# Optimization experiments

Measured on AMD Instinct MI355X. Metric: run time of the kernel, lower is better.

Reference implementation:

```python
import jax, jax.numpy as jnp
import numpy as np

B, N = 256, 256


def greedy_hard_perm(soft_perm):
    # soft_perm: (B, N, N). Sequential greedy masked-argmax assignment, vectorized over batch.
    Bn, Nn, _ = soft_perm.shape
    NEG = jnp.finfo(soft_perm.dtype).min
    b_idx = jnp.arange(Bn)

    def step(carry, _):
        scores, hard, row_mask, col_mask = carry
        # mask out already-assigned rows/cols (in-place masked_fill_ in torch -> carried scores)
        scores = jnp.where(row_mask[:, :, None], NEG, scores)
        scores = jnp.where(col_mask[:, None, :], NEG, scores)
        flat_idx = jnp.argmax(scores.reshape(Bn, -1), axis=1)  # (B,)
        r = flat_idx // Nn
        c = flat_idx % Nn
        hard = hard.at[b_idx, r, c].set(1.0)
        row_mask = row_mask.at[b_idx, r].set(True)
        col_mask = col_mask.at[b_idx, c].set(True)
        return (scores, hard, row_mask, col_mask), None

    init = (
        soft_perm,
        jnp.zeros_like(soft_perm),
        jnp.zeros((Bn, Nn), dtype=bool),
        jnp.zeros((Bn, Nn), dtype=bool),
    )
    (_, hard, _, _), _ = jax.lax.scan(step, init, None, length=Nn)
    return hard


def setup_inputs() -> dict:
    key = jax.random.key(0)
    logits = jax.random.normal(key, (B, N, N), dtype=jnp.float32)
    # realistic soft permutation: row-stochastic scores
    soft_perm = jax.nn.softmax(logits, axis=-1)
    return {"soft_perm": soft_perm}


def reference(soft_perm):
    # hard perm carries no gradient (built from constant 1.0 writes in torch)
    hard = greedy_hard_perm(jax.lax.stop_gradient(soft_perm))
    # straight-through estimator: forward = hard, backward = identity through soft
    return hard + soft_perm - jax.lax.stop_gradient(soft_perm)
```

## Files before the change

### kernel.cpp

```cpp
#include <hip/hip_runtime.h>
#include <math.h>

#define NEGINF (-INFINITY)

template <int CTRL>
__device__ __forceinline__ float dppmax(float x) {
    int xi = __float_as_int(x);
    int yi = __builtin_amdgcn_update_dpp(xi, xi, CTRL, 0xf, 0xf, false);
    return fmaxf(x, __int_as_float(yi));
}

__device__ __forceinline__ float wave_max64(float x) {
    x = dppmax<0x111>(x);
    x = dppmax<0x112>(x);
    x = dppmax<0x114>(x);
    x = dppmax<0x118>(x);
    x = dppmax<0x142>(x);
    x = dppmax<0x143>(x);
    return __int_as_float(__builtin_amdgcn_readlane(__float_as_int(x), 63));
}

__device__ __forceinline__ void wave_argmax(float v, int idx, float& out_v, int& out_idx) {
    float mv = wave_max64(v);
    unsigned long long mask = __ballot(v == mv);
    int ln = (int)__builtin_ctzll(mask);
    int bi = __builtin_amdgcn_readlane(idx, ln);
    unsigned long long rest = mask & (mask - 1);
    if (rest) {
        while (rest) {
            int l2 = (int)__builtin_ctzll(rest); rest &= rest - 1;
            int b2 = __builtin_amdgcn_readlane(idx, l2);
            if (b2 < bi) bi = b2;
        }
    }
    out_v = mv; out_idx = bi;
}

__global__ __launch_bounds__(64, 1) void greedy_perm_kernel(
        const float* __restrict__ soft, float* __restrict__ out) {
    const int b = blockIdx.x;
    const int lane = threadIdx.x;
    const size_t base = (size_t)b << 16;
    const float* sc = soft + base;
    float* ob = out + base;

    float v[4];
    int   c[4];

#pragma unroll
    for (int j = 0; j < 4; ++j) { v[j] = NEGINF; c[j] = 0; }

    const float4 zero4 = make_float4(0.f, 0.f, 0.f, 0.f);

    for (int k = 0; k < 64; k += 4) {
        float4 w[4][4];
#pragma unroll
        for (int j = 0; j < 4; ++j) {
            const float4* rp = (const float4*)(sc + (size_t)(j * 64 + lane) * 256);
#pragma unroll
            for (int kk = 0; kk < 4; ++kk) w[j][kk] = rp[k + kk];
        }
#pragma unroll
        for (int j = 0; j < 4; ++j) {
            float4* op = (float4*)(ob + (size_t)(j * 64 + lane) * 256);
#pragma unroll
            for (int kk = 0; kk < 4; ++kk) op[k + kk] = zero4;
        }
#pragma unroll
        for (int j = 0; j < 4; ++j) {
#pragma unroll
            for (int kk = 0; kk < 4; ++kk) {
                const float4 ww = w[j][kk];
                const int bc = 4 * (k + kk);
                if (ww.x > v[j]) { v[j] = ww.x; c[j] = bc + 0; }
                if (ww.y > v[j]) { v[j] = ww.y; c[j] = bc + 1; }
                if (ww.z > v[j]) { v[j] = ww.z; c[j] = bc + 2; }
                if (ww.w > v[j]) { v[j] = ww.w; c[j] = bc + 3; }
            }
        }
    }

    __threadfence_block();

    unsigned int colmask = 0;

    for (int step = 0; step < 256; ++step) {
        float bv = v[0];
        int   bf = (lane << 8) | (c[0] & 255);
#pragma unroll
        for (int j = 1; j < 4; ++j) {
            int f = ((j * 64 + lane) << 8) | (c[j] & 255);
            if (v[j] > bv || (v[j] == bv && f < bf)) { bv = v[j]; bf = f; }
        }
        float gv; int gf;
        wave_argmax(bv, bf, gv, gf);
        const int r  = gf >> 8;
        const int cc = gf & 255;

        if (lane == 0) ob[gf] = 1.0f;
        if (lane == (r & 63)) { v[r >> 6] = NEGINF; c[r >> 6] = 300; }
        if (lane == (cc >> 2)) colmask |= 1u << (cc & 3);

#pragma unroll
        for (int j = 0; j < 4; ++j) {
            unsigned long long m = __ballot(c[j] == cc);
            while (m) {
                const int ln = (int)__builtin_ctzll(m); m &= m - 1;
                const int row = j * 64 + ln;
                float4 w = *(const float4*)(sc + (size_t)row * 256 + lane * 4);
                float m0 = (colmask & 1u) ? NEGINF : w.x;
                float m1 = (colmask & 2u) ? NEGINF : w.y;
                float m2 = (colmask & 4u) ? NEGINF : w.z;
                float m3 = (colmask & 8u) ? NEGINF : w.w;
                float lv = m0; int lf = 4 * lane + 0;
                if (m1 > lv) { lv = m1; lf = 4 * lane + 1; }
                if (m2 > lv) { lv = m2; lf = 4 * lane + 2; }
                if (m3 > lv) { lv = m3; lf = 4 * lane + 3; }
                float rv; int rf;
                wave_argmax(lv, lf, rv, rf);
                if (lane == ln) { v[j] = rv; c[j] = rf; }
            }
        }
    }
}

extern "C" void kernel_launch(void* const* d_in, const int* in_sizes, int n_in,
                              void* d_out, int out_size, void* d_ws, size_t ws_size,
                              hipStream_t stream) {
    const float* soft = (const float*)d_in[0];
    float* out = (float*)d_out;
    const int n_batches = in_sizes[0] >> 16;

    greedy_perm_kernel<<<n_batches, 64, 0, stream>>>(soft, out);
}
```

Measured before the change: 327.7 us.

## Cache top-2 per row to skip rescans when best column is taken

```diff
diff --git a/kernel.cpp b/kernel.cpp
--- a/kernel.cpp
+++ b/kernel.cpp
@@ -2,6 +2,7 @@
 #include <math.h>
 
 #define NEGINF (-INFINITY)
+#define SENT 300
 
 template <int CTRL>
 __device__ __forceinline__ float dppmax(float x) {
@@ -38,17 +39,15 @@
 
 __global__ __launch_bounds__(64, 1) void greedy_perm_kernel(
         const float* __restrict__ soft, float* __restrict__ out) {
-    const int b = blockIdx.x;
     const int lane = threadIdx.x;
-    const size_t base = (size_t)b << 16;
+    const size_t base = (size_t)blockIdx.x << 16;
     const float* sc = soft + base;
     float* ob = out + base;
 
-    float v[4];
-    int   c[4];
-
+    float v1[4], v2[4];
+    int   c1[4], c2[4];
 #pragma unroll
-    for (int j = 0; j < 4; ++j) { v[j] = NEGINF; c[j] = 0; }
+    for (int j = 0; j < 4; ++j) { v1[j] = NEGINF; c1[j] = 0; v2[j] = NEGINF; c2[j] = 0; }
 
     const float4 zero4 = make_float4(0.f, 0.f, 0.f, 0.f);
 
@@ -71,54 +70,96 @@
 #pragma unroll
             for (int kk = 0; kk < 4; ++kk) {
                 const float4 ww = w[j][kk];
-                const int bc = 4 * (k + kk);
-                if (ww.x > v[j]) { v[j] = ww.x; c[j] = bc + 0; }
-                if (ww.y > v[j]) { v[j] = ww.y; c[j] = bc + 1; }
-                if (ww.z > v[j]) { v[j] = ww.z; c[j] = bc + 2; }
-                if (ww.w > v[j]) { v[j] = ww.w; c[j] = bc + 3; }
+                const float e[4] = {ww.x, ww.y, ww.z, ww.w};
+#pragma unroll
+                for (int q = 0; q < 4; ++q) {
+                    const float wv = e[q];
+                    const int   x  = 4 * (k + kk) + q;
+                    if (wv > v1[j])      { v2[j] = v1[j]; c2[j] = c1[j]; v1[j] = wv; c1[j] = x; }
+                    else if (wv > v2[j]) { v2[j] = wv; c2[j] = x; }
+                }
             }
         }
     }
-
     __threadfence_block();
 
-    unsigned int colmask = 0;
+    unsigned long long cm0 = 0, cm1 = 0, cm2 = 0, cm3 = 0;
 
     for (int step = 0; step < 256; ++step) {
-        float bv = v[0];
-        int   bf = (lane << 8) | (c[0] & 255);
+        float bv = v1[0]; int bf = (lane << 8) | (c1[0] & 255);
 #pragma unroll
         for (int j = 1; j < 4; ++j) {
-            int f = ((j * 64 + lane) << 8) | (c[j] & 255);
-            if (v[j] > bv || (v[j] == bv && f < bf)) { bv = v[j]; bf = f; }
+            int f = ((j * 64 + lane) << 8) | (c1[j] & 255);
+            if (v1[j] > bv || (v1[j] == bv && f < bf)) { bv = v1[j]; bf = f; }
         }
         float gv; int gf;
         wave_argmax(bv, bf, gv, gf);
-        const int r  = gf >> 8;
-        const int cc = gf & 255;
+        const int r = gf >> 8, cc = gf & 255;
 
-        if (lane == 0) ob[gf] = 1.0f;
-        if (lane == (r & 63)) { v[r >> 6] = NEGINF; c[r >> 6] = 300; }
-        if (lane == (cc >> 2)) colmask |= 1u << (cc & 3);
+        if (lane == 0) ob[(size_t)gf] = 1.0f;
+
+        {
+            const unsigned long long bit = 1ull << (cc & 63);
+            const int wsel = cc >> 6;
+            if (wsel == 0) cm0 |= bit; else if (wsel == 1) cm1 |= bit;
+            else if (wsel == 2) cm2 |= bit; else cm3 |= bit;
+        }
+#pragma unroll
+        for (int j = 0; j < 4; ++j)
+            if (r == j * 64 + lane) { v1[j] = NEGINF; c1[j] = SENT; v2[j] = NEGINF; c2[j] = SENT; }
+
+        unsigned need = 0;
+#pragma unroll
+        for (int j = 0; j < 4; ++j) {
+            if (c1[j] == cc) {
+                bool ok = false;
+                const int cx = c2[j];
+                if (cx != SENT) {
+                    const int ws = cx >> 6;
+                    const unsigned long long cw = ws == 0 ? cm0 : ws == 1 ? cm1 : ws == 2 ? cm2 : cm3;
+                    ok = ((cw >> (cx & 63)) & 1ull) == 0;
+                }
+                if (ok) { v1[j] = v2[j]; c1[j] = cx; v2[j] = NEGINF; c2[j] = SENT; }
+                else    need |= 1u << j;
+            }
+        }
 
 #pragma unroll
         for (int j = 0; j < 4; ++j) {
-            unsigned long long m = __ballot(c[j] == cc);
+            unsigned long long m = __ballot((need >> j) & 1u);
             while (m) {
                 const int ln = (int)__builtin_ctzll(m); m &= m - 1;
                 const int row = j * 64 + ln;
                 float4 w = *(const float4*)(sc + (size_t)row * 256 + lane * 4);
-                float m0 = (colmask & 1u) ? NEGINF : w.x;
-                float m1 = (colmask & 2u) ? NEGINF : w.y;
-                float m2 = (colmask & 4u) ? NEGINF : w.z;
-                float m3 = (colmask & 8u) ? NEGINF : w.w;
+                const int wsel = lane >> 4;
+                const unsigned long long cw = wsel == 0 ? cm0 : wsel == 1 ? cm1 : wsel == 2 ? cm2 : cm3;
+                const unsigned nib = (unsigned)(cw >> ((lane & 15) * 4)) & 15u;
+                float m0 = (nib & 1u) ? NEGINF : w.x;
+                float m1 = (nib & 2u) ? NEGINF : w.y;
+                float m2 = (nib & 4u) ? NEGINF : w.z;
+                float m3 = (nib & 8u) ? NEGINF : w.w;
                 float lv = m0; int lf = 4 * lane + 0;
                 if (m1 > lv) { lv = m1; lf = 4 * lane + 1; }
                 if (m2 > lv) { lv = m2; lf = 4 * lane + 2; }
                 if (m3 > lv) { lv = m3; lf = 4 * lane + 3; }
-                float rv; int rf;
-                wave_argmax(lv, lf, rv, rf);
-                if (lane == ln) { v[j] = rv; c[j] = rf; }
+                float rv1; int rf1;
+                wave_argmax(lv, lf, rv1, rf1);
+                if ((rf1 >> 2) == lane) {
+                    const int q = rf1 & 3;
+                    if (q == 0) m0 = NEGINF; else if (q == 1) m1 = NEGINF;
+                    else if (q == 2) m2 = NEGINF; else m3 = NEGINF;
+                }
+                lv = m0; lf = 4 * lane + 0;
+                if (m1 > lv) { lv = m1; lf = 4 * lane + 1; }
+                if (m2 > lv) { lv = m2; lf = 4 * lane + 2; }
+                if (m3 > lv) { lv = m3; lf = 4 * lane + 3; }
+                float rv2; int rf2;
+                wave_argmax(lv, lf, rv2, rf2);
+                if (lane == ln) {
+                    v1[j] = rv1; c1[j] = rf1;
+                    if (rv2 == NEGINF) { v2[j] = NEGINF; c2[j] = SENT; }
+                    else               { v2[j] = rv2;    c2[j] = rf2;  }
+                }
             }
         }
     }
@@ -130,6 +171,5 @@
     const float* soft = (const float*)d_in[0];
     float* out = (float*)d_out;
     const int n_batches = in_sizes[0] >> 16;
-
     greedy_perm_kernel<<<n_batches, 64, 0, stream>>>(soft, out);
 }
```

New measurement: 431.1 us. 31.6% more time.

## Defer stale-row rescans so row reloads overlap the next argmax step

Applied to the files above, without the earlier changes.

```diff
diff --git a/kernel.cpp b/kernel.cpp
--- a/kernel.cpp
+++ b/kernel.cpp
@@ -2,6 +2,8 @@
 #include <math.h>
 
 #define NEGINF (-INFINITY)
+#define C_STALE 256
+#define C_DEAD  511
 
 template <int CTRL>
 __device__ __forceinline__ float dppmax(float x) {
@@ -36,19 +38,34 @@
     out_v = mv; out_idx = bi;
 }
 
+__device__ __forceinline__ void consume_row(int row, float4 b, unsigned colmask,
+                                            int lane, float (&v1)[4], int (&c1)[4]) {
+    float m0 = (colmask & 1u) ? NEGINF : b.x;
+    float m1 = (colmask & 2u) ? NEGINF : b.y;
+    float m2 = (colmask & 4u) ? NEGINF : b.z;
+    float m3 = (colmask & 8u) ? NEGINF : b.w;
+    float lv = m0; int lf = 4 * lane + 0;
+    if (m1 > lv) { lv = m1; lf = 4 * lane + 1; }
+    if (m2 > lv) { lv = m2; lf = 4 * lane + 2; }
+    if (m3 > lv) { lv = m3; lf = 4 * lane + 3; }
+    float rv; int rf;
+    wave_argmax(lv, lf, rv, rf);
+    const int ow = row & 63, jj = row >> 6;
+#pragma unroll
+    for (int j2 = 0; j2 < 4; ++j2)
+        if (j2 == jj && lane == ow) { v1[j2] = rv; c1[j2] = rf; }
+}
+
 __global__ __launch_bounds__(64, 1) void greedy_perm_kernel(
         const float* __restrict__ soft, float* __restrict__ out) {
-    const int b = blockIdx.x;
     const int lane = threadIdx.x;
-    const size_t base = (size_t)b << 16;
+    const size_t base = (size_t)blockIdx.x << 16;
     const float* sc = soft + base;
     float* ob = out + base;
 
-    float v[4];
-    int   c[4];
-
+    float v1[4]; int c1[4];
 #pragma unroll
-    for (int j = 0; j < 4; ++j) { v[j] = NEGINF; c[j] = 0; }
+    for (int j = 0; j < 4; ++j) { v1[j] = NEGINF; c1[j] = 0; }
 
     const float4 zero4 = make_float4(0.f, 0.f, 0.f, 0.f);
 
@@ -72,54 +89,72 @@
             for (int kk = 0; kk < 4; ++kk) {
                 const float4 ww = w[j][kk];
                 const int bc = 4 * (k + kk);
-                if (ww.x > v[j]) { v[j] = ww.x; c[j] = bc + 0; }
-                if (ww.y > v[j]) { v[j] = ww.y; c[j] = bc + 1; }
-                if (ww.z > v[j]) { v[j] = ww.z; c[j] = bc + 2; }
-                if (ww.w > v[j]) { v[j] = ww.w; c[j] = bc + 3; }
+                if (ww.x > v1[j]) { v1[j] = ww.x; c1[j] = bc + 0; }
+                if (ww.y > v1[j]) { v1[j] = ww.y; c1[j] = bc + 1; }
+                if (ww.z > v1[j]) { v1[j] = ww.z; c1[j] = bc + 2; }
+                if (ww.w > v1[j]) { v1[j] = ww.w; c1[j] = bc + 3; }
             }
         }
     }
-
     __threadfence_block();
 
-    unsigned int colmask = 0;
+    unsigned colmask = 0;
+    int nstale = 0, srow0 = 0, srow1 = 0, srow2 = 0;
+    float4 b0 = zero4, b1 = zero4, b2 = zero4;
+    const int lsh = lane << 9;
 
     for (int step = 0; step < 256; ++step) {
-        float bv = v[0];
-        int   bf = (lane << 8) | (c[0] & 255);
+        float gv; int gf;
+        for (;;) {
+            float bv = v1[0]; int bf = lsh | c1[0];
 #pragma unroll
-        for (int j = 1; j < 4; ++j) {
-            int f = ((j * 64 + lane) << 8) | (c[j] & 255);
-            if (v[j] > bv || (v[j] == bv && f < bf)) { bv = v[j]; bf = f; }
+            for (int j = 1; j < 4; ++j) {
+                int f = (j << 15) | lsh | c1[j];
+                if (v1[j] > bv || (v1[j] == bv && f < bf)) { bv = v1[j]; bf = f; }
+            }
+            wave_argmax(bv, bf, gv, gf);
+            if ((gf & 511) != C_STALE) break;
+            if (nstale >= 1) consume_row(srow0, b0, colmask, lane, v1, c1);
+            if (nstale >= 2) consume_row(srow1, b1, colmask, lane, v1, c1);
+            if (nstale >= 3) consume_row(srow2, b2, colmask, lane, v1, c1);
+            nstale = 0;
         }
-        float gv; int gf;
-        wave_argmax(bv, bf, gv, gf);
-        const int r  = gf >> 8;
-        const int cc = gf & 255;
+        const int r = gf >> 9, cc = gf & 511;
 
-        if (lane == 0) ob[gf] = 1.0f;
-        if (lane == (r & 63)) { v[r >> 6] = NEGINF; c[r >> 6] = 300; }
+        if (lane == 0) ob[(size_t)r * 256 + cc] = 1.0f;
+        {
+            const int ow = r & 63, jw = r >> 6;
+#pragma unroll
+            for (int j2 = 0; j2 < 4; ++j2)
+                if (j2 == jw && lane == ow) { v1[j2] = NEGINF; c1[j2] = C_DEAD; }
+        }
         if (lane == (cc >> 2)) colmask |= 1u << (cc & 3);
 
+        if (nstale >= 1) consume_row(srow0, b0, colmask, lane, v1, c1);
+        if (nstale >= 2) consume_row(srow1, b1, colmask, lane, v1, c1);
+        if (nstale >= 3) consume_row(srow2, b2, colmask, lane, v1, c1);
+        nstale = 0;
+
+        if (step < 255) {
 #pragma unroll
-        for (int j = 0; j < 4; ++j) {
-            unsigned long long m = __ballot(c[j] == cc);
-            while (m) {
-                const int ln = (int)__builtin_ctzll(m); m &= m - 1;
-                const int row = j * 64 + ln;
-                float4 w = *(const float4*)(sc + (size_t)row * 256 + lane * 4);
-                float m0 = (colmask & 1u) ? NEGINF : w.x;
-                float m1 = (colmask & 2u) ? NEGINF : w.y;
-                float m2 = (colmask & 4u) ? NEGINF : w.z;
-                float m3 = (colmask & 8u) ? NEGINF : w.w;
-                float lv = m0; int lf = 4 * lane + 0;
-                if (m1 > lv) { lv = m1; lf = 4 * lane + 1; }
-                if (m2 > lv) { lv = m2; lf = 4 * lane + 2; }
-                if (m3 > lv) { lv = m3; lf = 4 * lane + 3; }
-                float rv; int rf;
-                wave_argmax(lv, lf, rv, rf);
-                if (lane == ln) { v[j] = rv; c[j] = rf; }
+            for (int j = 0; j < 4; ++j) {
+                unsigned long long m = __ballot(c1[j] == cc);
+                while (m) {
+                    const int ln = (int)__builtin_ctzll(m); m &= m - 1;
+                    const int row = j * 64 + ln;
+                    if (lane == ln) c1[j] = C_STALE;
+                    const float4* p = (const float4*)(sc + (size_t)row * 256 + lane * 4);
+                    if      (nstale == 0) { srow0 = row; b0 = *p; }
+                    else if (nstale == 1) { srow1 = row; b1 = *p; }
+                    else if (nstale == 2) { srow2 = row; b2 = *p; }
+                    else {
+                        float4 w = *p;
+                        consume_row(row, w, colmask, lane, v1, c1);
+                    }
+                    ++nstale;
+                }
             }
+            if (nstale > 3) nstale = 3;
         }
     }
 }
@@ -130,6 +165,5 @@
     const float* soft = (const float*)d_in[0];
     float* out = (float*)d_out;
     const int n_batches = in_sizes[0] >> 16;
-
     greedy_perm_kernel<<<n_batches, 64, 0, stream>>>(soft, out);
 }
```

After: 424.3 us. 29.5% more time.

## Track top-two per row and use packed 64-bit keys for argmax

Applied to the files above, without the earlier changes.

```diff
diff --git a/kernel.cpp b/kernel.cpp
--- a/kernel.cpp
+++ b/kernel.cpp
@@ -3,122 +3,156 @@
 
 #define NEGINF (-INFINITY)
 
+
 template <int CTRL>
-__device__ __forceinline__ float dppmax(float x) {
-    int xi = __float_as_int(x);
-    int yi = __builtin_amdgcn_update_dpp(xi, xi, CTRL, 0xf, 0xf, false);
-    return fmaxf(x, __int_as_float(yi));
+__device__ __forceinline__ void dppmax_key(unsigned& h, unsigned& l) {
+    unsigned oh = (unsigned)__builtin_amdgcn_update_dpp((int)h, (int)h, CTRL, 0xf, 0xf, false);
+    unsigned ol = (unsigned)__builtin_amdgcn_update_dpp((int)l, (int)l, CTRL, 0xf, 0xf, false);
+    unsigned long long a = ((unsigned long long)h << 32) | l;
+    unsigned long long b = ((unsigned long long)oh << 32) | ol;
+    if (b > a) { h = oh; l = ol; }
 }
 
-__device__ __forceinline__ float wave_max64(float x) {
-    x = dppmax<0x111>(x);
-    x = dppmax<0x112>(x);
-    x = dppmax<0x114>(x);
-    x = dppmax<0x118>(x);
-    x = dppmax<0x142>(x);
-    x = dppmax<0x143>(x);
-    return __int_as_float(__builtin_amdgcn_readlane(__float_as_int(x), 63));
+__device__ __forceinline__ void wave_max_key(unsigned& h, unsigned& l) {
+    dppmax_key<0x111>(h, l);
+    dppmax_key<0x112>(h, l);
+    dppmax_key<0x114>(h, l);
+    dppmax_key<0x118>(h, l);
+    dppmax_key<0x142>(h, l);
+    dppmax_key<0x143>(h, l);
+    h = (unsigned)__builtin_amdgcn_readlane((int)h, 63);
+    l = (unsigned)__builtin_amdgcn_readlane((int)l, 63);
 }
 
-__device__ __forceinline__ void wave_argmax(float v, int idx, float& out_v, int& out_idx) {
-    float mv = wave_max64(v);
-    unsigned long long mask = __ballot(v == mv);
-    int ln = (int)__builtin_ctzll(mask);
-    int bi = __builtin_amdgcn_readlane(idx, ln);
-    unsigned long long rest = mask & (mask - 1);
-    if (rest) {
-        while (rest) {
-            int l2 = (int)__builtin_ctzll(rest); rest &= rest - 1;
-            int b2 = __builtin_amdgcn_readlane(idx, l2);
-            if (b2 < bi) bi = b2;
-        }
-    }
-    out_v = mv; out_idx = bi;
+__device__ __forceinline__ void take_key(unsigned& bh, unsigned& bl, unsigned h, unsigned l) {
+    unsigned long long a = ((unsigned long long)bh << 32) | bl;
+    unsigned long long b = ((unsigned long long)h << 32) | l;
+    if (b > a) { bh = h; bl = l; }
 }
 
 __global__ __launch_bounds__(64, 1) void greedy_perm_kernel(
         const float* __restrict__ soft, float* __restrict__ out) {
-    const int b = blockIdx.x;
     const int lane = threadIdx.x;
-    const size_t base = (size_t)b << 16;
+    const size_t base = (size_t)blockIdx.x << 16;
     const float* sc = soft + base;
     float* ob = out + base;
 
-    float v[4];
-    int   c[4];
+    unsigned k1h[4], k1l[4], k2h[4], k2l[4];
 
+    {
+        float v1[4], v2[4]; int c1[4], c2[4];
 #pragma unroll
-    for (int j = 0; j < 4; ++j) { v[j] = NEGINF; c[j] = 0; }
-
-    const float4 zero4 = make_float4(0.f, 0.f, 0.f, 0.f);
-
-    for (int k = 0; k < 64; k += 4) {
-        float4 w[4][4];
+        for (int j = 0; j < 4; ++j) { v1[j] = NEGINF; c1[j] = 0; v2[j] = NEGINF; c2[j] = 0; }
+        const float4 zero4 = make_float4(0.f, 0.f, 0.f, 0.f);
+        for (int k = 0; k < 64; k += 4) {
+            float4 w[4][4];
 #pragma unroll
-        for (int j = 0; j < 4; ++j) {
-            const float4* rp = (const float4*)(sc + (size_t)(j * 64 + lane) * 256);
+            for (int j = 0; j < 4; ++j) {
+                const float4* rp = (const float4*)(sc + (size_t)(j * 64 + lane) * 256);
 #pragma unroll
-            for (int kk = 0; kk < 4; ++kk) w[j][kk] = rp[k + kk];
+                for (int kk = 0; kk < 4; ++kk) w[j][kk] = rp[k + kk];
+            }
+#pragma unroll
+            for (int j = 0; j < 4; ++j) {
+                float4* op = (float4*)(ob + (size_t)(j * 64 + lane) * 256);
+#pragma unroll
+                for (int kk = 0; kk < 4; ++kk) op[k + kk] = zero4;
+            }
+#pragma unroll
+            for (int j = 0; j < 4; ++j) {
+#pragma unroll
+                for (int kk = 0; kk < 4; ++kk) {
+                    const float4 ww = w[j][kk];
+                    const float e[4] = {ww.x, ww.y, ww.z, ww.w};
+#pragma unroll
+                    for (int q = 0; q < 4; ++q) {
+                        const float wv = e[q];
+                        const int   x  = 4 * (k + kk) + q;
+                        if (wv > v1[j])      { v2[j] = v1[j]; c2[j] = c1[j]; v1[j] = wv; c1[j] = x; }
+                        else if (wv > v2[j]) { v2[j] = wv; c2[j] = x; }
+                    }
+                }
+            }
         }
 #pragma unroll
         for (int j = 0; j < 4; ++j) {
-            float4* op = (float4*)(ob + (size_t)(j * 64 + lane) * 256);
-#pragma unroll
-            for (int kk = 0; kk < 4; ++kk) op[k + kk] = zero4;
-        }
-#pragma unroll
-        for (int j = 0; j < 4; ++j) {
-#pragma unroll
-            for (int kk = 0; kk < 4; ++kk) {
-                const float4 ww = w[j][kk];
-                const int bc = 4 * (k + kk);
-                if (ww.x > v[j]) { v[j] = ww.x; c[j] = bc + 0; }
-                if (ww.y > v[j]) { v[j] = ww.y; c[j] = bc + 1; }
-                if (ww.z > v[j]) { v[j] = ww.z; c[j] = bc + 2; }
-                if (ww.w > v[j]) { v[j] = ww.w; c[j] = bc + 3; }
-            }
+            const unsigned rsh = (unsigned)((j * 64 + lane) << 8);
+            k1h[j] = __float_as_uint(v1[j]); k1l[j] = ~(rsh | (unsigned)c1[j]);
+            k2h[j] = __float_as_uint(v2[j]); k2l[j] = ~(rsh | (unsigned)c2[j]);
         }
     }
-
     __threadfence_block();
 
-    unsigned int colmask = 0;
+    unsigned nib = 0;
+    unsigned long long cm0 = 0, cm1 = 0, cm2 = 0, cm3 = 0;
 
     for (int step = 0; step < 256; ++step) {
-        float bv = v[0];
-        int   bf = (lane << 8) | (c[0] & 255);
+        unsigned bh = k1h[0], bl = k1l[0];
+        take_key(bh, bl, k1h[1], k1l[1]);
+        take_key(bh, bl, k1h[2], k1l[2]);
+        take_key(bh, bl, k1h[3], k1l[3]);
+        wave_max_key(bh, bl);
+        const unsigned flat = (~bl) & 0xFFFFu;
+        const int r = (int)(flat >> 8), cc = (int)(flat & 255u);
+
+        if (lane == 0) ob[flat] = 1.0f;
+
+        {
+            const int jw = r >> 6, ow = r & 63;
 #pragma unroll
-        for (int j = 1; j < 4; ++j) {
-            int f = ((j * 64 + lane) << 8) | (c[j] & 255);
-            if (v[j] > bv || (v[j] == bv && f < bf)) { bv = v[j]; bf = f; }
+            for (int j = 0; j < 4; ++j)
+                if (j == jw && lane == ow) { k1h[j] = 0; k1l[j] = 0; k2h[j] = 0; k2l[j] = 0; }
         }
-        float gv; int gf;
-        wave_argmax(bv, bf, gv, gf);
-        const int r  = gf >> 8;
-        const int cc = gf & 255;
+        if (lane == (cc >> 2)) nib |= 1u << (cc & 3);
+        if      (cc < 64)  cm0 |= 1ull << cc;
+        else if (cc < 128) cm1 |= 1ull << (cc - 64);
+        else if (cc < 192) cm2 |= 1ull << (cc - 128);
+        else               cm3 |= 1ull << (cc - 192);
 
-        if (lane == 0) ob[gf] = 1.0f;
-        if (lane == (r & 63)) { v[r >> 6] = NEGINF; c[r >> 6] = 300; }
-        if (lane == (cc >> 2)) colmask |= 1u << (cc & 3);
+        if (step == 255) break;
 
 #pragma unroll
         for (int j = 0; j < 4; ++j) {
-            unsigned long long m = __ballot(c[j] == cc);
+            unsigned long long m =
+                __ballot(k1h[j] != 0u && (((~k1l[j]) & 255u) == (unsigned)cc));
             while (m) {
                 const int ln = (int)__builtin_ctzll(m); m &= m - 1;
                 const int row = j * 64 + ln;
-                float4 w = *(const float4*)(sc + (size_t)row * 256 + lane * 4);
-                float m0 = (colmask & 1u) ? NEGINF : w.x;
-                float m1 = (colmask & 2u) ? NEGINF : w.y;
-                float m2 = (colmask & 4u) ? NEGINF : w.z;
-                float m3 = (colmask & 8u) ? NEGINF : w.w;
-                float lv = m0; int lf = 4 * lane + 0;
-                if (m1 > lv) { lv = m1; lf = 4 * lane + 1; }
-                if (m2 > lv) { lv = m2; lf = 4 * lane + 2; }
-                if (m3 > lv) { lv = m3; lf = 4 * lane + 3; }
-                float rv; int rf;
-                wave_argmax(lv, lf, rv, rf);
-                if (lane == ln) { v[j] = rv; c[j] = rf; }
+                const unsigned q2h = (unsigned)__builtin_amdgcn_readlane((int)k2h[j], ln);
+                const unsigned q2l = (unsigned)__builtin_amdgcn_readlane((int)k2l[j], ln);
+                bool promote = false;
+                if (q2h != 0u) {
+                    const int c2 = (int)((~q2l) & 255u);
+                    const unsigned long long cw =
+                        c2 < 64 ? cm0 : c2 < 128 ? cm1 : c2 < 192 ? cm2 : cm3;
+                    promote = ((cw >> (c2 & 63)) & 1ull) == 0ull;
+                }
+                if (promote) {
+                    if (lane == ln) { k1h[j] = q2h; k1l[j] = q2l; k2h[j] = 0; k2l[j] = 0; }
+                } else {
+                    float4 w = *(const float4*)(sc + (size_t)row * 256 + lane * 4);
+                    const unsigned lbase = ~((unsigned)(row << 8) | (unsigned)(4 * lane));
+                    unsigned eh[4], el[4];
+                    eh[0] = (nib & 1u) ? 0u : __float_as_uint(w.x); el[0] = lbase - 0u;
+                    eh[1] = (nib & 2u) ? 0u : __float_as_uint(w.y); el[1] = lbase - 1u;
+                    eh[2] = (nib & 4u) ? 0u : __float_as_uint(w.z); el[2] = lbase - 2u;
+                    eh[3] = (nib & 8u) ? 0u : __float_as_uint(w.w); el[3] = lbase - 3u;
+                    unsigned ah = eh[0], al = el[0];
+                    take_key(ah, al, eh[1], el[1]);
+                    take_key(ah, al, eh[2], el[2]);
+                    take_key(ah, al, eh[3], el[3]);
+                    wave_max_key(ah, al);
+                    const int c1w = (int)((~al) & 255u), qq = c1w & 3;
+#pragma unroll
+                    for (int q = 0; q < 4; ++q)
+                        if (q == qq && lane == (c1w >> 2)) { eh[q] = 0; el[q] = 0; }
+                    unsigned sh = eh[0], sl = el[0];
+                    take_key(sh, sl, eh[1], el[1]);
+                    take_key(sh, sl, eh[2], el[2]);
+                    take_key(sh, sl, eh[3], el[3]);
+                    wave_max_key(sh, sl);
+                    if (lane == ln) { k1h[j] = ah; k1l[j] = al; k2h[j] = sh; k2l[j] = sl; }
+                }
             }
         }
     }
@@ -130,6 +164,5 @@
     const float* soft = (const float*)d_in[0];
     float* out = (float*)d_out;
     const int n_batches = in_sizes[0] >> 16;
-
     greedy_perm_kernel<<<n_batches, 64, 0, stream>>>(soft, out);
 }
```

Result: slower. 415.2 us (+26.7%).
